# Performance work log

Measured on AMD Instinct MI355X. Metric: run time of the kernel, lower is better.

Reference implementation:

```python
import jax, jax.numpy as jnp
import numpy as np
import math

B, L, D = 2, 2048, 1024
H, DH, R, MAX_ORDER = 16, 64, 512, 5
NUM_BASIS = MAX_ORDER + 1  # min(basis_rank=512, 6)


def setup_inputs() -> dict:
    key = jax.random.key(0)
    ks = jax.random.split(key, 8)
    s = 0.02
    return {
        "hidden_states": jax.random.normal(ks[0], (B, L, D), jnp.float32),
        "attention_mask": jnp.zeros((B, 1, 1, L), jnp.float32),
        "Wq": jax.random.normal(ks[1], (D, D), jnp.float32) * s,
        "bq": jnp.zeros((D,), jnp.float32),
        "Wk": jax.random.normal(ks[2], (D, D), jnp.float32) * s,
        "bk": jnp.zeros((D,), jnp.float32),
        "Wv": jax.random.normal(ks[3], (D, D), jnp.float32) * s,
        "bv": jnp.zeros((D,), jnp.float32),
        "q_proj_weight": jax.random.normal(ks[4], (H, DH, R), jnp.float32) / math.sqrt(DH),
        "k_proj_weight": jax.random.normal(ks[5], (H, DH, R), jnp.float32) / math.sqrt(DH),
        "coefficients": jax.random.normal(ks[6], (H, NUM_BASIS), jnp.float32) * s,
    }


def _basis_bias(coefficients, seq_len, dtype):
    # rel[i, j] = (j - i) / (L - 1), clamped to [-1, 1]; DCT basis cos(pi * k * x)
    pos = jnp.arange(seq_len, dtype=dtype)
    x = jnp.clip((pos[None, :] - pos[:, None]) / max(seq_len - 1, 1), -1.0, 1.0)
    k = jnp.arange(NUM_BASIS, dtype=dtype)
    tk = jnp.cos(jnp.pi * x[..., None] * k)  # [L, L, K]
    return jnp.einsum('hk,ijk->hij', coefficients, tk)  # [H, L, L]


def reference(hidden_states, attention_mask, Wq, bq, Wk, bk, Wv, bv,
              q_proj_weight, k_proj_weight, coefficients):
    b, l, _ = hidden_states.shape

    def shape_heads(x):
        return x.reshape(b, l, H, DH).transpose(0, 2, 1, 3)  # [B, H, L, DH]

    q = shape_heads(hidden_states @ Wq.T + bq)
    k = shape_heads(hidden_states @ Wk.T + bk)
    v = shape_heads(hidden_states @ Wv.T + bv)

    qp = jnp.einsum('bhld,hdr->bhlr', q, q_proj_weight)
    kp = jnp.einsum('bhld,hdr->bhlr', k, k_proj_weight)
    scores = jnp.einsum('bhlr,bhmr->bhlm', qp, kp) / math.sqrt(R)

    bias = _basis_bias(coefficients, l, scores.dtype)
    scores = scores + bias[None] + attention_mask

    probs = jax.nn.softmax(scores, axis=-1)  # dropout is identity in eval
    ctx = jnp.einsum('bhlm,bhmd->bhld', probs, v)
    return ctx.transpose(0, 2, 1, 3).reshape(b, l, H * DH)
```

## Files before the change

kernel.cpp:

```cpp
#include <hip/hip_runtime.h>


typedef unsigned short ushort_t;
typedef __attribute__((ext_vector_type(8))) short bf16x8;
typedef __attribute__((ext_vector_type(4))) float f32x4;

#define LOG2E 1.4426950408889634f

__device__ inline f32x4 mfma16(bf16x8 a, bf16x8 b, f32x4 c) {
  return __builtin_amdgcn_mfma_f32_16x16x32_bf16(a, b, c, 0, 0, 0);
}
__device__ inline void load_lds16(const void* g, void* l) {
  __builtin_amdgcn_global_load_lds((const __attribute__((address_space(1))) unsigned int*)g,
                                   (__attribute__((address_space(3))) unsigned int*)l, 16, 0, 0);
}
__device__ inline ushort_t f2bf(float f) {
  union { float f; unsigned int u; } v; v.f = f;
  unsigned int u = v.u;
  return (ushort_t)((u + 0x7fffu + ((u >> 16) & 1u)) >> 16);
}
__device__ inline unsigned cvt_pk_bf16(float lo, float hi) {
  unsigned r;
  asm("v_cvt_pk_bf16_f32 %0, %1, %2" : "=v"(r) : "v"(lo), "v"(hi));
  return r;
}
#if __has_builtin(__builtin_amdgcn_exp2f)
__device__ inline float exp2_(float x) { return __builtin_amdgcn_exp2f(x); }
#else
__device__ inline float exp2_(float x) { return exp2f(x); }
#endif

__global__ __launch_bounds__(256) void k_pre0(
    const float* __restrict__ kpw, const float* __restrict__ coef,
    const float* __restrict__ maskp,
    float* __restrict__ kpwT, float* __restrict__ tab, float* __restrict__ mask2) {
  const int blk = blockIdx.x, tid = threadIdx.x;
  if (blk < 128) {
    __shared__ float tile[64][65];
    int h = blk >> 3, rt = blk & 7;
    const float* src = kpw + ((size_t)h * 64) * 512 + rt * 64;
    #pragma unroll
    for (int i = 0; i < 4; i++) {
      int idx = i * 256 + tid;
      int row = idx >> 4, c4 = idx & 15;
      float4 v = *(const float4*)(src + (size_t)row * 512 + c4 * 4);
      *(float4*)(&tile[row][c4 * 4]) = v;
    }
    __syncthreads();
    float* dst = kpwT + ((size_t)h * 512 + rt * 64) * 64;
    #pragma unroll
    for (int i = 0; i < 4; i++) {
      int idx = i * 256 + tid;
      int r = idx >> 4, c4 = idx & 15;
      float4 v = {tile[c4 * 4 + 0][r], tile[c4 * 4 + 1][r],
                  tile[c4 * 4 + 2][r], tile[c4 * 4 + 3][r]};
      *(float4*)(dst + (size_t)r * 64 + c4 * 4) = v;
    }
  } else if (blk < 384) {
    int local = blk - 128;
    int h = local >> 4, t = (local & 15) * 256 + tid;
    if (t < 4095) {
      float x = (float)(t - 2047) * (1.0f / 2047.0f);
      float s = 0.f;
      #pragma unroll
      for (int k = 0; k < 6; k++)
        s += coef[h * 6 + k] * cosf(3.14159265358979323846f * (float)k * x);
      tab[h * 4095 + t] = s * LOG2E;
    }
  } else {
    int i = (blk - 384) * 256 + tid;
    if (i < 4096) mask2[i] = maskp[i] * LOG2E;
  }
}

__global__ __launch_bounds__(256) void k_prep(
    const float* __restrict__ hidden, const float* __restrict__ Wk,
    const float* __restrict__ Wv, const float* __restrict__ qpw,
    const float* __restrict__ kpwT,
    ushort_t* __restrict__ hb, ushort_t* __restrict__ w3, float* __restrict__ Ah) {
  const int blk = blockIdx.x, tid = threadIdx.x;
  if (blk < 64) {
    int h = blk >> 2, db = (blk & 3) * 16;
    int dp = tid & 63, d0 = db + (tid >> 6) * 4;
    float acc[4] = {0.f, 0.f, 0.f, 0.f};
    const float* kT = kpwT + (size_t)h * 512 * 64 + dp;
    const float* qr = qpw + ((size_t)h * 64 + d0) * 512;
    for (int r = 0; r < 512; r += 4) {
      float4 wk = {kT[(size_t)(r + 0) * 64], kT[(size_t)(r + 1) * 64],
                   kT[(size_t)(r + 2) * 64], kT[(size_t)(r + 3) * 64]};
      #pragma unroll
      for (int i = 0; i < 4; i++) {
        float4 wq = *(const float4*)(qr + i * 512 + r);
        acc[i] += wq.x * wk.x + wq.y * wk.y + wq.z * wk.z + wq.w * wk.w;
      }
    }
    #pragma unroll
    for (int i = 0; i < 4; i++)
      Ah[((size_t)h * 64 + d0 + i) * 64 + dp] = acc[i] * (0.044194173824159216f * LOG2E);
  } else {
    const float* in;
    ushort_t* out;
    int base = blk - 64;
    if (base < 4096) { in = hidden; out = hb; }
    else if (base < 5120) { in = Wk; out = w3 + 1048576; base -= 4096; }
    else { in = Wv; out = w3 + 2097152; base -= 5120; }
    int i = (base * 256 + tid) * 4;
    float4 v = *(const float4*)(in + i);
    unsigned long long pk = (unsigned long long)f2bf(v.x)
                          | ((unsigned long long)f2bf(v.y) << 16)
                          | ((unsigned long long)f2bf(v.z) << 32)
                          | ((unsigned long long)f2bf(v.w) << 48);
    *(unsigned long long*)(out + i) = pk;
  }
}

__global__ __launch_bounds__(256) void k_wq(
    const float* __restrict__ Wq, const float* __restrict__ Ah,
    const float* __restrict__ bq, ushort_t* __restrict__ w3, float* __restrict__ bq2) {
  __shared__ float wq_s[64][65];
  __shared__ float ah_s[64][65];
  int h = blockIdx.y, ct = blockIdx.x;
  int t = threadIdx.x;
  #pragma unroll
  for (int i = 0; i < 16; i++) {
    int idx = i * 256 + t, r = idx >> 6, c = idx & 63;
    wq_s[r][c] = Wq[((size_t)h * 64 + r) * 1024 + ct * 64 + c];
    ah_s[r][c] = Ah[((size_t)h * 64 + r) * 64 + c];
  }
  __syncthreads();
  int dp = t >> 2, cg = (t & 3) * 16;
  float acc[16];
  #pragma unroll
  for (int j = 0; j < 16; j++) acc[j] = 0.f;
  for (int d = 0; d < 64; d++) {
    float a = ah_s[d][dp];
    #pragma unroll
    for (int j = 0; j < 16; j++) acc[j] += a * wq_s[d][cg + j];
  }
  ushort_t* orow = w3 + ((size_t)h * 64 + dp) * 1024 + ct * 64 + cg;
  #pragma unroll
  for (int j = 0; j < 16; j += 4) {
    unsigned long long pk = (unsigned long long)f2bf(acc[j])
                          | ((unsigned long long)f2bf(acc[j + 1]) << 16)
                          | ((unsigned long long)f2bf(acc[j + 2]) << 32)
                          | ((unsigned long long)f2bf(acc[j + 3]) << 48);
    *(unsigned long long*)(orow + j) = pk;
  }
  if (ct == 0 && t < 64) {
    float bsum = 0.f;
    for (int d = 0; d < 64; d++) bsum += bq[h * 64 + d] * ah_s[d][t];
    bq2[h * 64 + t] = bsum;
  }
}

__global__ __launch_bounds__(256) void k_gemm(
    const ushort_t* __restrict__ hb, const ushort_t* __restrict__ w3,
    const float* __restrict__ bq2, const float* __restrict__ bk,
    const float* __restrict__ bv, ushort_t* __restrict__ qk, ushort_t* __restrict__ vT) {
  __shared__ ushort_t Asm[128 * 32];
  __shared__ ushort_t Bsm[128 * 32];
  const int tid = threadIdx.x, w = tid >> 6, l = tid & 63, g = l >> 4, l15 = l & 15;
  const int raw = blockIdx.x;
  const int id = (raw & 7) * 96 + (raw >> 3);
  const bool isv = id >= 512;
  int bx, by;
  const ushort_t *Aptr, *Bptr;
  if (!isv) { bx = id & 31; by = id >> 5; Aptr = hb; Bptr = w3; }
  else { int id2 = id - 512; bx = id2 & 7; by = id2 >> 3; Aptr = w3 + 2048 * 1024; Bptr = hb; }
  const int mbase = bx * 128, nbase = by * 128;
  const int wrow = (w >> 1) * 64, wcol = (w & 1) * 64;
  f32x4 zero4 = {0.f, 0.f, 0.f, 0.f};
  f32x4 acc[4][4];
  #pragma unroll
  for (int i = 0; i < 4; i++)
    #pragma unroll
    for (int j = 0; j < 4; j++) acc[i][j] = zero4;

  for (int kt = 0; kt < 32; ++kt) {
    __syncthreads();
    #pragma unroll
    for (int i = 0; i < 2; i++) {
      int inst = w * 2 + i;
      int r = inst * 16 + (l >> 2);
      int cs = (l & 3) ^ (r & 3);
      load_lds16(Aptr + (size_t)(mbase + r) * 1024 + kt * 32 + cs * 8, &Asm[inst * 512]);
      load_lds16(Bptr + (size_t)(nbase + r) * 1024 + kt * 32 + cs * 8, &Bsm[inst * 512]);
    }
    __syncthreads();
    bf16x8 a[4], bfr[4];
    #pragma unroll
    for (int rt = 0; rt < 4; rt++) {
      int r = wrow + rt * 16 + l15;
      a[rt] = *(const bf16x8*)(&Asm[r * 32 + ((g ^ (r & 3)) << 3)]);
    }
    #pragma unroll
    for (int ct = 0; ct < 4; ct++) {
      int r = wcol + ct * 16 + l15;
      bfr[ct] = *(const bf16x8*)(&Bsm[r * 32 + ((g ^ (r & 3)) << 3)]);
    }
    #pragma unroll
    for (int rt = 0; rt < 4; rt++)
      #pragma unroll
      for (int ct = 0; ct < 4; ct++)
        acc[rt][ct] = mfma16(a[rt], bfr[ct], acc[rt][ct]);
  }
  if (!isv) {
    #pragma unroll
    for (int ct = 0; ct < 4; ct++) {
      int n = nbase + wcol + ct * 16 + l15;
      float bias = (n < 1024) ? bq2[n] : bk[n - 1024];
      #pragma unroll
      for (int rt = 0; rt < 4; rt++)
        #pragma unroll
        for (int reg = 0; reg < 4; reg++) {
          int m = mbase + wrow + rt * 16 + g * 4 + reg;
          qk[(size_t)m * 2048 + n] = f2bf(acc[rt][ct][reg] + bias);
        }
    }
  } else {
    #pragma unroll
    for (int rt = 0; rt < 4; rt++)
      #pragma unroll
      for (int reg = 0; reg < 4; reg++) {
        int dg = mbase + wrow + rt * 16 + g * 4 + reg;
        float bias = bv[dg];
        ushort_t* vrow = vT + ((size_t)(dg >> 6)) * 131072 + (size_t)(dg & 63) * 2048;
        #pragma unroll
        for (int ct = 0; ct < 4; ct++) {
          int mg = nbase + wcol + ct * 16 + l15;
          vrow[((size_t)(mg >> 11)) * 2097152 + (mg & 2047)] = f2bf(acc[rt][ct][reg] + bias);
        }
      }
  }
}

__global__ __launch_bounds__(256, 4) void k_attn(
    const ushort_t* __restrict__ qk, const ushort_t* __restrict__ vT,
    const float* __restrict__ tab, const float* __restrict__ mask2,
    float* __restrict__ out) {
  __shared__ ushort_t k_sm[2][64][64];
  __shared__ ushort_t vt_sm[2][64][64];
  const int tid = threadIdx.x, w = tid >> 6, l = tid & 63, g = l >> 4, l15 = l & 15;
  const int e01 = l15 & 3, a0 = (l15 >> 2) & 1;
  const int lr = l >> 3, lc = l & 7;
  const int bid = blockIdx.x, xcd = bid & 7, slot = bid >> 3;
  const int bh = xcd * 4 + (slot & 3), qb = slot >> 2;
  const int b = bh >> 4, h = bh & 15;
  const int wrow = qb * 64 + w * 16;
  const int q = wrow + l15;

  const ushort_t* kbase = qk + 1024 + h * 64;
  const ushort_t* vT_bh = vT + (size_t)bh * 64 * 2048;
  const float* tabh = tab + h * 4095 + 2047;
  const float* maskb = mask2 + b * 2048;

  auto stage = [&](int t, int bi) {
    int kvb = t * 64;
    #pragma unroll
    for (int ii = 0; ii < 2; ii++) {
      int m = w * 16 + ii * 8 + lr;
      int sc = lc ^ ((lr & 3) | (ii << 2));
      load_lds16(kbase + (size_t)(b * 2048 + kvb + m) * 2048 + sc * 8,
                 &k_sm[bi][w * 16 + ii * 8][0]);
    }
    #pragma unroll
    for (int ii = 0; ii < 2; ii++) {
      int d = w * 16 + ii * 8 + lr;
      int sc = lc ^ ((lr & 3) | (ii << 2));
      load_lds16(vT_bh + (size_t)d * 2048 + kvb + sc * 8,
                 &vt_sm[bi][w * 16 + ii * 8][0]);
    }
  };

  stage(0, 0);

  bf16x8 qf[2];
  {
    const ushort_t* qpr = qk + (size_t)(b * 2048 + q) * 2048 + h * 64 + g * 8;
    qf[0] = *(const bf16x8*)(qpr);
    qf[1] = *(const bf16x8*)(qpr + 32);
  }

  f32x4 zero4 = {0.f, 0.f, 0.f, 0.f};
  f32x4 ctx[4];
  float lrow = 0.f;
  #pragma unroll
  for (int dt = 0; dt < 4; dt++) ctx[dt] = zero4;

  __syncthreads();

  for (int t = 0; t < 32; t++) {
    const int bi = t & 1;
    const int kvb = t * 64;
    if (t < 31) stage(t + 1, bi ^ 1);

    f32x4 ST[4];
    #pragma unroll
    for (int mt = 0; mt < 4; mt++) ST[mt] = zero4;
    #pragma unroll
    for (int ks = 0; ks < 2; ks++) {
      #pragma unroll
      for (int mt = 0; mt < 4; mt++) {
        int mr = (mt >> 1) * 32 + (l15 >> 2) * 8 + (mt & 1) * 4 + e01;
        int pc = (ks * 4 + g) ^ (e01 | (a0 << 2));
        bf16x8 af = *(const bf16x8*)(&k_sm[bi][mr][pc * 8]);
        ST[mt] = mfma16(af, qf[ks], ST[mt]);
      }
    }

    float pv[4][4];
    #pragma unroll
    for (int mt = 0; mt < 4; mt++) {
      int mo = kvb + (mt >> 1) * 32 + g * 8 + (mt & 1) * 4;
      float4 mk = *(const float4*)(maskb + mo);
      const float* tq = tabh + mo - q;
      pv[mt][0] = exp2_(ST[mt][0] + mk.x + tq[0]);
      pv[mt][1] = exp2_(ST[mt][1] + mk.y + tq[1]);
      pv[mt][2] = exp2_(ST[mt][2] + mk.z + tq[2]);
      pv[mt][3] = exp2_(ST[mt][3] + mk.w + tq[3]);
      lrow += pv[mt][0] + pv[mt][1] + pv[mt][2] + pv[mt][3];
    }
    bf16x8 pf[2];
    {
      union { unsigned u[4]; bf16x8 v; } pk0, pk1;
      pk0.u[0] = cvt_pk_bf16(pv[0][0], pv[0][1]);
      pk0.u[1] = cvt_pk_bf16(pv[0][2], pv[0][3]);
      pk0.u[2] = cvt_pk_bf16(pv[1][0], pv[1][1]);
      pk0.u[3] = cvt_pk_bf16(pv[1][2], pv[1][3]);
      pk1.u[0] = cvt_pk_bf16(pv[2][0], pv[2][1]);
      pk1.u[1] = cvt_pk_bf16(pv[2][2], pv[2][3]);
      pk1.u[2] = cvt_pk_bf16(pv[3][0], pv[3][1]);
      pk1.u[3] = cvt_pk_bf16(pv[3][2], pv[3][3]);
      pf[0] = pk0.v;
      pf[1] = pk1.v;
    }

    #pragma unroll
    for (int kp = 0; kp < 2; kp++) {
      #pragma unroll
      for (int dt = 0; dt < 4; dt++) {
        int d = dt * 16 + l15;
        int pc = (kp * 4 + g) ^ (e01 | (((l15 >> 3) & 1) << 2));
        bf16x8 vf = *(const bf16x8*)(&vt_sm[bi][d][pc * 8]);
        ctx[dt] = mfma16(vf, pf[kp], ctx[dt]);
      }
    }

    __syncthreads();
  }

  lrow += __shfl_xor(lrow, 16);
  lrow += __shfl_xor(lrow, 32);
  float inv = 1.0f / lrow;
  float* op = out + ((size_t)(b * 2048 + q)) * 1024 + h * 64 + g * 4;
  #pragma unroll
  for (int dt = 0; dt < 4; dt++) {
    float4 o = {ctx[dt][0] * inv, ctx[dt][1] * inv, ctx[dt][2] * inv, ctx[dt][3] * inv};
    *(float4*)(op + dt * 16) = o;
  }
}

extern "C" void kernel_launch(void* const* d_in, const int* in_sizes, int n_in,
                              void* d_out, int out_size, void* d_ws, size_t ws_size,
                              hipStream_t stream) {
  const float* hidden = (const float*)d_in[0];
  const float* maskp  = (const float*)d_in[1];
  const float* Wq     = (const float*)d_in[2];
  const float* bq     = (const float*)d_in[3];
  const float* Wk     = (const float*)d_in[4];
  const float* bk     = (const float*)d_in[5];
  const float* Wv     = (const float*)d_in[6];
  const float* bv     = (const float*)d_in[7];
  const float* qpw    = (const float*)d_in[8];
  const float* kpw    = (const float*)d_in[9];
  const float* coef   = (const float*)d_in[10];

  char* ws = (char*)d_ws;
  float*    tab   = (float*)(ws);
  ushort_t* hb    = (ushort_t*)(ws + 262144);
  ushort_t* w3    = (ushort_t*)(ws + 8650752);
  float*    Ah    = (float*)(ws + 14942208);
  float*    bq2   = (float*)(ws + 15204352);
  float*    mask2 = (float*)(ws + 15208448);
  ushort_t* qkb   = (ushort_t*)(ws + 15224832);
  ushort_t* vTb   = (ushort_t*)(ws + 32002048);
  float*    kpwT  = (float*)(ws + 40390656);

  k_pre0<<<400, 256, 0, stream>>>(kpw, coef, maskp, kpwT, tab, mask2);
  k_prep<<<6208, 256, 0, stream>>>(hidden, Wk, Wv, qpw, kpwT, hb, w3, Ah);
  k_wq<<<dim3(16, 16), 256, 0, stream>>>(Wq, Ah, bq, w3, bq2);
  k_gemm<<<768, 256, 0, stream>>>(hb, w3, bq2, bk, bv, qkb, vTb);
  k_attn<<<1024, 256, 0, stream>>>(qkb, vTb, tab, mask2, (float*)d_out);
}
```

Baseline: 158.3 us.

## Fold DCT position bias and mask into an extra MFMA via cos/sin expansion

Expands cos(pi*k*(m-q)/(L-1)) as cos*cos+sin*sin, so the per-head relative-position bias becomes a rank-11 dot product between per-query and per-key feature vectors. The mask is carried as one extra key column, padded to a 32-wide bf16 K dimension. The attention kernel stages these key features into LDS and adds one MFMA per tile, replacing the gather from the bias table and mask with pure exp2. The trade-off is that bias and mask are now rounded to bf16, which adds error, and the attention kernel gains extra LDS traffic and MFMA work.

New measurement: 146.6 us. 1.08x faster.

```diff
diff --git a/kernel.cpp b/kernel.cpp
--- a/kernel.cpp
+++ b/kernel.cpp
@@ -2,10 +2,12 @@
 
 
 typedef unsigned short ushort_t;
+typedef unsigned long long ull_t;
 typedef __attribute__((ext_vector_type(8))) short bf16x8;
 typedef __attribute__((ext_vector_type(4))) float f32x4;
 
 #define LOG2E 1.4426950408889634f
+#define PI_F 3.14159265358979323846f
 
 __device__ inline f32x4 mfma16(bf16x8 a, bf16x8 b, f32x4 c) {
   return __builtin_amdgcn_mfma_f32_16x16x32_bf16(a, b, c, 0, 0, 0);
@@ -33,7 +35,7 @@
 __global__ __launch_bounds__(256) void k_pre0(
     const float* __restrict__ kpw, const float* __restrict__ coef,
     const float* __restrict__ maskp,
-    float* __restrict__ kpwT, float* __restrict__ tab, float* __restrict__ mask2) {
+    float* __restrict__ kpwT, ushort_t* __restrict__ ke, ushort_t* __restrict__ qe) {
   const int blk = blockIdx.x, tid = threadIdx.x;
   if (blk < 128) {
     __shared__ float tile[64][65];
@@ -56,20 +58,53 @@
                   tile[c4 * 4 + 2][r], tile[c4 * 4 + 3][r]};
       *(float4*)(dst + (size_t)r * 64 + c4 * 4) = v;
     }
-  } else if (blk < 384) {
-    int local = blk - 128;
-    int h = local >> 4, t = (local & 15) * 256 + tid;
-    if (t < 4095) {
-      float x = (float)(t - 2047) * (1.0f / 2047.0f);
-      float s = 0.f;
-      #pragma unroll
-      for (int k = 0; k < 6; k++)
-        s += coef[h * 6 + k] * cosf(3.14159265358979323846f * (float)k * x);
-      tab[h * 4095 + t] = s * LOG2E;
+  } else if (blk < 144) {
+    int i = (blk - 128) * 256 + tid;
+    int bb = i >> 11, m = i & 2047;
+    float base = PI_F * (float)m * (1.0f / 2047.0f);
+    ushort_t row[32];
+    row[0] = f2bf(1.0f);
+    #pragma unroll
+    for (int k = 1; k <= 5; k++) {
+      float a = base * (float)k;
+      row[2 * k - 1] = f2bf(cosf(a));
+      row[2 * k]     = f2bf(sinf(a));
+    }
+    row[11] = f2bf(maskp[bb * 2048 + m] * LOG2E);
+    #pragma unroll
+    for (int j = 12; j < 32; j++) row[j] = 0;
+    ull_t* dst = (ull_t*)(ke + ((size_t)(bb * 2048 + m)) * 32);
+    #pragma unroll
+    for (int j = 0; j < 4; j++) {
+      ull_t pk = 0;
+      #pragma unroll
+      for (int e = 0; e < 4; e++) pk |= (ull_t)row[j * 4 + e] << (16 * e);
+      dst[j] = pk;
     }
   } else {
-    int i = (blk - 384) * 256 + tid;
-    if (i < 4096) mask2[i] = maskp[i] * LOG2E;
+    int i = (blk - 144) * 256 + tid;
+    int h = i >> 11, q = i & 2047;
+    float base = PI_F * (float)q * (1.0f / 2047.0f);
+    ushort_t row[32];
+    row[0] = f2bf(coef[h * 6] * LOG2E);
+    #pragma unroll
+    for (int k = 1; k <= 5; k++) {
+      float ck = coef[h * 6 + k] * LOG2E;
+      float a = base * (float)k;
+      row[2 * k - 1] = f2bf(ck * cosf(a));
+      row[2 * k]     = f2bf(ck * sinf(a));
+    }
+    row[11] = f2bf(1.0f);
+    #pragma unroll
+    for (int j = 12; j < 32; j++) row[j] = 0;
+    ull_t* dst = (ull_t*)(qe + ((size_t)(h * 2048 + q)) * 32);
+    #pragma unroll
+    for (int j = 0; j < 4; j++) {
+      ull_t pk = 0;
+      #pragma unroll
+      for (int e = 0; e < 4; e++) pk |= (ull_t)row[j * 4 + e] << (16 * e);
+      dst[j] = pk;
+    }
   }
 }
 
@@ -236,10 +271,11 @@
 
 __global__ __launch_bounds__(256, 4) void k_attn(
     const ushort_t* __restrict__ qk, const ushort_t* __restrict__ vT,
-    const float* __restrict__ tab, const float* __restrict__ mask2,
+    const ushort_t* __restrict__ qe, const ushort_t* __restrict__ ke,
     float* __restrict__ out) {
   __shared__ ushort_t k_sm[2][64][64];
   __shared__ ushort_t vt_sm[2][64][64];
+  __shared__ ushort_t ke_sm[2][64][32];
   const int tid = threadIdx.x, w = tid >> 6, l = tid & 63, g = l >> 4, l15 = l & 15;
   const int e01 = l15 & 3, a0 = (l15 >> 2) & 1;
   const int lr = l >> 3, lc = l & 7;
@@ -251,8 +287,7 @@
 
   const ushort_t* kbase = qk + 1024 + h * 64;
   const ushort_t* vT_bh = vT + (size_t)bh * 64 * 2048;
-  const float* tabh = tab + h * 4095 + 2047;
-  const float* maskb = mask2 + b * 2048;
+  const ushort_t* ke_b = ke + (size_t)b * 2048 * 32;
 
   auto stage = [&](int t, int bi) {
     int kvb = t * 64;
@@ -270,15 +305,21 @@
       load_lds16(vT_bh + (size_t)d * 2048 + kvb + sc * 8,
                  &vt_sm[bi][w * 16 + ii * 8][0]);
     }
+    {
+      int ml = l >> 2, c = l & 3;
+      load_lds16(ke_b + (size_t)(kvb + w * 16 + ml) * 32 + ((c ^ (ml & 3)) << 3),
+                 &ke_sm[bi][w * 16][0]);
+    }
   };
 
   stage(0, 0);
 
-  bf16x8 qf[2];
+  bf16x8 qf[2], qfe;
   {
     const ushort_t* qpr = qk + (size_t)(b * 2048 + q) * 2048 + h * 64 + g * 8;
     qf[0] = *(const bf16x8*)(qpr);
     qf[1] = *(const bf16x8*)(qpr + 32);
+    qfe = *(const bf16x8*)(qe + ((size_t)(h * 2048 + q)) * 32 + g * 8);
   }
 
   f32x4 zero4 = {0.f, 0.f, 0.f, 0.f};
@@ -291,7 +332,6 @@
 
   for (int t = 0; t < 32; t++) {
     const int bi = t & 1;
-    const int kvb = t * 64;
     if (t < 31) stage(t + 1, bi ^ 1);
 
     f32x4 ST[4];
@@ -307,17 +347,20 @@
         ST[mt] = mfma16(af, qf[ks], ST[mt]);
       }
     }
+    #pragma unroll
+    for (int mt = 0; mt < 4; mt++) {
+      int mr = (mt >> 1) * 32 + (l15 >> 2) * 8 + (mt & 1) * 4 + e01;
+      bf16x8 af = *(const bf16x8*)(&ke_sm[bi][mr][(g ^ e01) * 8]);
+      ST[mt] = mfma16(af, qfe, ST[mt]);
+    }
 
     float pv[4][4];
     #pragma unroll
     for (int mt = 0; mt < 4; mt++) {
-      int mo = kvb + (mt >> 1) * 32 + g * 8 + (mt & 1) * 4;
-      float4 mk = *(const float4*)(maskb + mo);
-      const float* tq = tabh + mo - q;
-      pv[mt][0] = exp2_(ST[mt][0] + mk.x + tq[0]);
-      pv[mt][1] = exp2_(ST[mt][1] + mk.y + tq[1]);
-      pv[mt][2] = exp2_(ST[mt][2] + mk.z + tq[2]);
-      pv[mt][3] = exp2_(ST[mt][3] + mk.w + tq[3]);
+      pv[mt][0] = exp2_(ST[mt][0]);
+      pv[mt][1] = exp2_(ST[mt][1]);
+      pv[mt][2] = exp2_(ST[mt][2]);
+      pv[mt][3] = exp2_(ST[mt][3]);
       lrow += pv[mt][0] + pv[mt][1] + pv[mt][2] + pv[mt][3];
     }
     bf16x8 pf[2];
@@ -376,19 +419,19 @@
   const float* coef   = (const float*)d_in[10];
 
   char* ws = (char*)d_ws;
-  float*    tab   = (float*)(ws);
+  ushort_t* keb   = (ushort_t*)(ws);
   ushort_t* hb    = (ushort_t*)(ws + 262144);
   ushort_t* w3    = (ushort_t*)(ws + 8650752);
   float*    Ah    = (float*)(ws + 14942208);
   float*    bq2   = (float*)(ws + 15204352);
-  float*    mask2 = (float*)(ws + 15208448);
-  ushort_t* qkb   = (ushort_t*)(ws + 15224832);
-  ushort_t* vTb   = (ushort_t*)(ws + 32002048);
-  float*    kpwT  = (float*)(ws + 40390656);
-
-  k_pre0<<<400, 256, 0, stream>>>(kpw, coef, maskp, kpwT, tab, mask2);
+  ushort_t* qeb   = (ushort_t*)(ws + 15208448);
+  ushort_t* qkb   = (ushort_t*)(ws + 17305600);
+  ushort_t* vTb   = (ushort_t*)(ws + 34082816);
+  float*    kpwT  = (float*)(ws + 42471424);
+
+  k_pre0<<<272, 256, 0, stream>>>(kpw, coef, maskp, kpwT, keb, qeb);
   k_prep<<<6208, 256, 0, stream>>>(hidden, Wk, Wv, qpw, kpwT, hb, w3, Ah);
   k_wq<<<dim3(16, 16), 256, 0, stream>>>(Wq, Ah, bq, w3, bq2);
   k_gemm<<<768, 256, 0, stream>>>(hb, w3, bq2, bk, bv, qkb, vTb);
-  k_attn<<<1024, 256, 0, stream>>>(qkb, vTb, tab, mask2, (float*)d_out);
-}
+  k_attn<<<1024, 256, 0, stream>>>(qkb, vTb, qeb, keb, (float*)d_out);
+}
```
